# Kernel optimization log

Measured on AMD Instinct MI355X. Metric: run time of the kernel, lower is better.

## Reference

```python
import jax, jax.numpy as jnp
import numpy as np

N0, N1, N2 = 100000, 50000, 25000
E0, E1 = 400000, 200000
H1, D1 = 4, 64   # layer0: 4 heads x 64
H2, D2 = 1, 64   # layer1: 1 head  x 64
SLOPE = 0.2      # DGL GATConv leaky_relu negative_slope


def gat_conv(h_src, h_dst, src, dst, W, attn_l, attn_r, bias, n_dst, heads, d):
    # linear projection (shared between src and dst, as in DGL GATConv)
    f_src = (h_src @ W).reshape(-1, heads, d)   # (N_src, H, D)
    f_dst = (h_dst @ W).reshape(-1, heads, d)   # (N_dst, H, D)
    el = jnp.einsum('nhd,hd->nh', f_src, attn_l)  # (N_src, H)
    er = jnp.einsum('nhd,hd->nh', f_dst, attn_r)  # (N_dst, H)
    e = jax.nn.leaky_relu(el[src] + er[dst], SLOPE)  # (E, H)
    # edge-softmax over incoming edges of each dst node (numerically stable)
    m = jax.ops.segment_max(e, dst, num_segments=n_dst)      # (N_dst, H)
    ee = jnp.exp(e - m[dst])
    s = jax.ops.segment_sum(ee, dst, num_segments=n_dst)
    alpha = ee / s[dst]                                      # (E, H)
    msg = f_src[src] * alpha[:, :, None]                     # (E, H, D)
    out = jax.ops.segment_sum(msg, dst, num_segments=n_dst)  # (N_dst, H, D)
    return out + bias.reshape(1, heads, d)


def setup_inputs() -> dict:
    key = jax.random.key(0)
    ks = jax.random.split(key, 12)
    return {
        'x': jax.random.normal(ks[0], (N0, 256), jnp.float32),
        'e0_src': jax.random.randint(ks[1], (E0,), 0, N0, jnp.int32),
        'e0_dst': jax.random.randint(ks[2], (E0,), 0, N1, jnp.int32),
        'e1_src': jax.random.randint(ks[3], (E1,), 0, N1, jnp.int32),
        'e1_dst': jax.random.randint(ks[4], (E1,), 0, N2, jnp.int32),
        'W1': jax.random.normal(ks[5], (256, H1 * D1), jnp.float32) * 0.06,
        'al1': jax.random.normal(ks[6], (H1, D1), jnp.float32) * 0.1,
        'ar1': jax.random.normal(ks[7], (H1, D1), jnp.float32) * 0.1,
        'b1': jnp.zeros((H1 * D1,), jnp.float32),
        'W2': jax.random.normal(ks[8], (H1 * D1, H2 * D2), jnp.float32) * 0.06,
        'al2': jax.random.normal(ks[9], (H2, D2), jnp.float32) * 0.1,
        'ar2': jax.random.normal(ks[10], (H2, D2), jnp.float32) * 0.1,
        'b2': jnp.zeros((H2 * D2,), jnp.float32),
    }


def reference(x, e0_src, e0_dst, e1_src, e1_dst,
              W1, al1, ar1, b1, W2, al2, ar2, b2):
    # layer 0: block 100k src -> 50k dst; dst nodes are a prefix of src nodes
    h = gat_conv(x, x[:N1], e0_src, e0_dst, W1, al1, ar1, b1, N1, H1, D1)
    h = jax.nn.relu(h).reshape(N1, H1 * D1)   # activation + flatten(1); dropout is identity at eval
    # layer 1 (final): single head, no activation, flatten
    h = gat_conv(h, h[:N2], e1_src, e1_dst, W2, al2, ar2, b2, N2, H2, D2)
    return h.reshape(N2, H2 * D2)
```

## Files before the change

### kernel.cpp

```cpp
#include <hip/hip_runtime.h>
#include <cstddef>
#include <cstdint>

constexpr int cN0 = 100000, cN1 = 50000, cN2 = 25000;
constexpr int cE0 = 400000, cE1 = 200000;
constexpr float SLOPE = 0.2f;

typedef short short8  __attribute__((ext_vector_type(8)));
typedef short short4v __attribute__((ext_vector_type(4)));
typedef float f32x4   __attribute__((ext_vector_type(4)));

__device__ __forceinline__ unsigned short f2bf(float x) {
    union { float f; uint32_t u; } c; c.f = x;
    uint32_t u = c.u + 0x7FFFu + ((c.u >> 16) & 1u);
    return (unsigned short)(u >> 16);
}
__device__ __forceinline__ float bf2f(uint32_t u) {
    union { uint32_t u; float f; } c; c.u = u << 16; return c.f;
}
__device__ __forceinline__ float lrelu(float x) { return x >= 0.f ? x : SLOPE * x; }

__device__ __forceinline__ uint32_t cvtpk(float lo, float hi) {
    uint32_t r;
    asm("v_cvt_pk_bf16_f32 %0, %1, %2" : "=v"(r) : "v"(lo), "v"(hi));
    return r;
}

__device__ __forceinline__ void gload_lds16(const void* g, void* l) {
    __builtin_amdgcn_global_load_lds(
        (const __attribute__((address_space(1))) unsigned int*)g,
        (__attribute__((address_space(3))) unsigned int*)l, 16, 0, 0);
}


__global__ void hist2_kernel(const int* __restrict__ d0, const int* __restrict__ d1,
                             int* __restrict__ cnt0, int* __restrict__ cnt1) {
    int i = blockIdx.x * blockDim.x + threadIdx.x;
    if (i < cE0) atomicAdd(&cnt0[d0[i]], 1);
    int j = i - cE0;
    if (j >= 0 && j < cE1) atomicAdd(&cnt1[d1[j]], 1);
}

__global__ __launch_bounds__(256) void chunk_sum2_kernel(const int* __restrict__ cnt0, int n0,
                                                         const int* __restrict__ cnt1, int n1,
                                                         int* __restrict__ bsum0, int* __restrict__ bsum1,
                                                         int nblk1) {
    const int* cnt = blockIdx.y ? cnt1 : cnt0;
    int n = blockIdx.y ? n1 : n0;
    int* bsum = blockIdx.y ? bsum1 : bsum0;
    if (blockIdx.y && (int)blockIdx.x >= nblk1) return;
    int i = blockIdx.x * 256 + threadIdx.x;
    int v = (i < n) ? cnt[i] : 0;
    #pragma unroll
    for (int o = 32; o; o >>= 1) v += __shfl_xor(v, o);
    __shared__ int ws[4];
    if ((threadIdx.x & 63) == 0) ws[threadIdx.x >> 6] = v;
    __syncthreads();
    if (threadIdx.x == 0) bsum[blockIdx.x] = ws[0] + ws[1] + ws[2] + ws[3];
}

__device__ __forceinline__ int block_exscan(int v, int& total) {
    int lane = threadIdx.x & 63, w = threadIdx.x >> 6;
    int x = v;
    #pragma unroll
    for (int o = 1; o < 64; o <<= 1) { int t = __shfl_up(x, o); if (lane >= o) x += t; }
    __shared__ int ws[4];
    if (lane == 63) ws[w] = x;
    __syncthreads();
    int add = 0;
    #pragma unroll
    for (int i = 0; i < 4; ++i) if (i < w) add += ws[i];
    total = ws[0] + ws[1] + ws[2] + ws[3];
    return add + x - v;
}

__global__ __launch_bounds__(256) void top_scan2_kernel(const int* __restrict__ bsum0, int nblk0,
                                                        const int* __restrict__ bsum1, int nblk1,
                                                        int* __restrict__ boff0, int* __restrict__ boff1,
                                                        int* __restrict__ tot0, int* __restrict__ tot1) {
    int i = threadIdx.x;
    int tot;
    int v = (i < nblk0) ? bsum0[i] : 0;
    int e = block_exscan(v, tot);
    if (i < nblk0) boff0[i] = e;
    if (i == 0) *tot0 = tot;
    __syncthreads();
    v = (i < nblk1) ? bsum1[i] : 0;
    e = block_exscan(v, tot);
    if (i < nblk1) boff1[i] = e;
    if (i == 0) *tot1 = tot;
}

__global__ __launch_bounds__(256) void chunk_scan2_kernel(const int* __restrict__ cnt0, int n0,
                                                          const int* __restrict__ cnt1, int n1,
                                                          const int* __restrict__ boff0, const int* __restrict__ boff1,
                                                          int* __restrict__ offs0, int* __restrict__ cursor0,
                                                          int* __restrict__ offs1, int* __restrict__ cursor1,
                                                          int nblk1) {
    const int* cnt = blockIdx.y ? cnt1 : cnt0;
    const int* boff = blockIdx.y ? boff1 : boff0;
    int* offs = blockIdx.y ? offs1 : offs0;
    int* cursor = blockIdx.y ? cursor1 : cursor0;
    int n = blockIdx.y ? n1 : n0;
    if (blockIdx.y && (int)blockIdx.x >= nblk1) return;
    int i = blockIdx.x * 256 + threadIdx.x;
    int v = (i < n) ? cnt[i] : 0;
    int tot; int e = block_exscan(v, tot) + boff[blockIdx.x];
    if (i < n) { offs[i] = e; cursor[i] = e; }
}

__global__ void scatter2_kernel(const int* __restrict__ s0, const int* __restrict__ d0,
                                const int* __restrict__ s1, const int* __restrict__ d1,
                                int* __restrict__ cursor0, int* __restrict__ srcidx0,
                                int* __restrict__ cursor1, int* __restrict__ srcidx1) {
    int i = blockIdx.x * blockDim.x + threadIdx.x;
    if (i < cE0) { int p = atomicAdd(&cursor0[d0[i]], 1); srcidx0[p] = s0[i]; }
    int j = i - cE0;
    if (j >= 0 && j < cE1) { int p = atomicAdd(&cursor1[d1[j]], 1); srcidx1[p] = s1[j]; }
}

__global__ __launch_bounds__(256) void bf16_transpose2_kernel(const float* __restrict__ W1,
                                                              const float* __restrict__ W2,
                                                              short* __restrict__ bt1,
                                                              short* __restrict__ bt2) {
    int i = blockIdx.x * 256 + threadIdx.x;
    if (i < 256 * 256) {
        int k = i >> 8, n = i & 255;
        bt1[(size_t)n * 256 + k] = (short)f2bf(W1[i]);
    } else {
        int j = i - 256 * 256;
        if (j < 256 * 64) {
            int k = j >> 6, n = j & 63;
            bt2[(size_t)n * 256 + k] = (short)f2bf(W2[j]);
        }
    }
}

__global__ __launch_bounds__(512, 2) void gemm0_breg(
    const float* __restrict__ A, const short* __restrict__ BT,
    unsigned short* __restrict__ C,
    const float* __restrict__ al, const float* __restrict__ ar,
    float* __restrict__ el, float* __restrict__ er,
    int M, int erN)
{
    __shared__ short Bs[256 * 256];

    const int tid = threadIdx.x;
    const int w = tid >> 6;
    const int lane = tid & 63;
    const int ln = lane & 15;
    const int kg = lane >> 4;
    const int m0 = blockIdx.x * 256;

    #pragma unroll
    for (int i = 0; i < 16; ++i) {
        int seg = 2 * (i * 8 + w);
        int r = seg + (lane >> 5);
        int c = (lane & 31) ^ (r & 7);
        gload_lds16(&BT[(size_t)r * 256 + c * 8], &Bs[(size_t)seg * 256]);
    }

    f32x4 acc[2][16];
    #pragma unroll
    for (int mi = 0; mi < 2; ++mi)
        #pragma unroll
        for (int ni = 0; ni < 16; ++ni)
            #pragma unroll
            for (int j = 0; j < 4; ++j) acc[mi][ni][j] = 0.f;

    int r0 = m0 + w * 32 + ln;      if (r0 >= M) r0 = M - 1;
    int r1 = m0 + w * 32 + 16 + ln; if (r1 >= M) r1 = M - 1;
    const float* ap0 = A + (size_t)r0 * 256 + kg * 8;
    const float* ap1 = A + (size_t)r1 * 256 + kg * 8;

    float4 pa[2][2][2];
    auto loadA = [&](int kt, int buf) {
        pa[buf][0][0] = *(const float4*)(ap0 + kt * 32);
        pa[buf][0][1] = *(const float4*)(ap0 + kt * 32 + 4);
        pa[buf][1][0] = *(const float4*)(ap1 + kt * 32);
        pa[buf][1][1] = *(const float4*)(ap1 + kt * 32 + 4);
    };

    loadA(0, 0);
    __syncthreads();

    const int swb = ln & 7;
    #pragma unroll
    for (int kt = 0; kt < 8; ++kt) {
        const int buf = kt & 1;
        if (kt + 1 < 8) loadA(kt + 1, buf ^ 1);
        short8 af[2];
        #pragma unroll
        for (int mi = 0; mi < 2; ++mi) {
            const float4 p0 = pa[buf][mi][0];
            const float4 p1 = pa[buf][mi][1];
            union { uint32_t u[4]; short8 s; } cv;
            cv.u[0] = cvtpk(p0.x, p0.y);
            cv.u[1] = cvtpk(p0.z, p0.w);
            cv.u[2] = cvtpk(p1.x, p1.y);
            cv.u[3] = cvtpk(p1.z, p1.w);
            af[mi] = cv.s;
        }
        #pragma unroll
        for (int ni = 0; ni < 16; ++ni) {
            int row = ni * 16 + ln;
            int pc = (kt * 4 + kg) ^ swb;
            short8 bf = *(const short8*)&Bs[row * 256 + pc * 8];
            acc[0][ni] = __builtin_amdgcn_mfma_f32_16x16x32_bf16(af[0], bf, acc[0][ni], 0, 0, 0);
            acc[1][ni] = __builtin_amdgcn_mfma_f32_16x16x32_bf16(af[1], bf, acc[1][ni], 0, 0, 0);
        }
    }

    float alv[16], arv[16];
    #pragma unroll
    for (int ni = 0; ni < 16; ++ni) {
        alv[ni] = al[ni * 16 + ln];
        arv[ni] = ar[ni * 16 + ln];
    }
    #pragma unroll
    for (int mi = 0; mi < 2; ++mi) {
        #pragma unroll
        for (int j = 0; j < 4; ++j) {
            float pl[4] = {0, 0, 0, 0}, pr[4] = {0, 0, 0, 0};
            #pragma unroll
            for (int ni = 0; ni < 16; ++ni) {
                float v = acc[mi][ni][j];
                pl[ni >> 2] += v * alv[ni];
                pr[ni >> 2] += v * arv[ni];
            }
            #pragma unroll
            for (int h = 0; h < 4; ++h)
                #pragma unroll
                for (int o = 1; o < 16; o <<= 1) {
                    pl[h] += __shfl_xor(pl[h], o);
                    pr[h] += __shfl_xor(pr[h], o);
                }
            int row = m0 + w * 32 + mi * 16 + kg * 4 + j;
            if (row < M) {
                #pragma unroll
                for (int ni = 0; ni < 16; ++ni)
                    C[(size_t)row * 256 + ni * 16 + ln] = f2bf(acc[mi][ni][j]);
                if (ln == 0) {
                    #pragma unroll
                    for (int h = 0; h < 4; ++h) {
                        el[row * 4 + h] = pl[h];
                        if (row < erN) er[row * 4 + h] = pr[h];
                    }
                }
            }
        }
    }
}

template<int BM, int BN, int WR, int WC>
__global__ __launch_bounds__(256) void gemm_bf16_fused(
    const unsigned short* __restrict__ A, const short* __restrict__ BT,
    unsigned short* __restrict__ C,
    const float* __restrict__ al, const float* __restrict__ ar,
    float* __restrict__ el, float* __restrict__ er,
    int M, int K, int nh, int erN)
{
    constexpr int BK = 32;
    constexpr int PITCH = BK + 8;
    constexpr int MI = BM / WR / 16;
    constexpr int NI = BN / WC / 16;
    constexpr int AITB = BM * 4 / 256;
    constexpr int BIT  = BN * 4 / 256;

    __shared__ short As[BM * PITCH];
    __shared__ short Bs[BN * PITCH];

    const int tid = threadIdx.x;
    const int w = tid >> 6;
    const int lane = tid & 63;
    const int ln = lane & 15;
    const int kg = lane >> 4;
    const int wr = w / WC;
    const int wc = w % WC;
    const int m0 = blockIdx.x * BM;
    const int n0 = blockIdx.y * BN;
    const int N = nh * 64;

    f32x4 acc[MI][NI];
    #pragma unroll
    for (int mi = 0; mi < MI; ++mi)
        #pragma unroll
        for (int ni = 0; ni < NI; ++ni)
            #pragma unroll
            for (int j = 0; j < 4; ++j) acc[mi][ni][j] = 0.f;

    short8 aregb[AITB];
    short8 breg[BIT];

    auto loadA = [&](int k0) {
        #pragma unroll
        for (int p = 0; p < AITB; ++p) {
            int slot = tid + p * 256;
            int r = slot >> 2;
            int kq = (slot & 3) * 8;
            int gr = m0 + r;
            short8 v = {};
            if (gr < M) v = *(const short8*)&A[(size_t)gr * K + k0 + kq];
            aregb[p] = v;
        }
    };
    auto loadB = [&](int k0) {
        #pragma unroll
        for (int p = 0; p < BIT; ++p) {
            int slot = tid + p * 256;
            int r = slot >> 2;
            int kq = (slot & 3) * 8;
            breg[p] = *(const short8*)&BT[(size_t)(n0 + r) * K + k0 + kq];
        }
    };
    auto writeLDS = [&]() {
        #pragma unroll
        for (int p = 0; p < AITB; ++p) {
            int slot = tid + p * 256;
            int r = slot >> 2;
            int kq = (slot & 3) * 8;
            *(short8*)&As[r * PITCH + kq] = aregb[p];
        }
        #pragma unroll
        for (int p = 0; p < BIT; ++p) {
            int slot = tid + p * 256;
            int r = slot >> 2;
            int kq = (slot & 3) * 8;
            *(short8*)&Bs[r * PITCH + kq] = breg[p];
        }
    };

    loadA(0); loadB(0);
    const int T = K / BK;
    for (int t = 0; t < T; ++t) {
        writeLDS();
        __syncthreads();
        if (t + 1 < T) { loadA((t + 1) * BK); loadB((t + 1) * BK); }
        short8 af[MI], bf[NI];
        #pragma unroll
        for (int mi = 0; mi < MI; ++mi)
            af[mi] = *(const short8*)&As[(wr * MI * 16 + mi * 16 + ln) * PITCH + kg * 8];
        #pragma unroll
        for (int ni = 0; ni < NI; ++ni)
            bf[ni] = *(const short8*)&Bs[(wc * NI * 16 + ni * 16 + ln) * PITCH + kg * 8];
        #pragma unroll
        for (int mi = 0; mi < MI; ++mi)
            #pragma unroll
            for (int ni = 0; ni < NI; ++ni)
                acc[mi][ni] = __builtin_amdgcn_mfma_f32_16x16x32_bf16(af[mi], bf[ni], acc[mi][ni], 0, 0, 0);
        __syncthreads();
    }

    const int h = (n0 + wc * NI * 16) >> 6;
    float alv[NI], arv[NI];
    #pragma unroll
    for (int ni = 0; ni < NI; ++ni) {
        alv[ni] = al[h * 64 + ni * 16 + ln];
        arv[ni] = ar[h * 64 + ni * 16 + ln];
    }
    #pragma unroll
    for (int mi = 0; mi < MI; ++mi) {
        float pl[4] = {0, 0, 0, 0}, pr[4] = {0, 0, 0, 0};
        #pragma unroll
        for (int ni = 0; ni < NI; ++ni)
            #pragma unroll
            for (int j = 0; j < 4; ++j) {
                float v = acc[mi][ni][j];
                pl[j] += v * alv[ni];
                pr[j] += v * arv[ni];
            }
        #pragma unroll
        for (int j = 0; j < 4; ++j)
            #pragma unroll
            for (int o = 1; o < 16; o <<= 1) {
                pl[j] += __shfl_xor(pl[j], o);
                pr[j] += __shfl_xor(pr[j], o);
            }
        #pragma unroll
        for (int j = 0; j < 4; ++j) {
            int row = m0 + wr * MI * 16 + mi * 16 + kg * 4 + j;
            if (row < M) {
                #pragma unroll
                for (int ni = 0; ni < NI; ++ni)
                    C[(size_t)row * N + n0 + wc * NI * 16 + ni * 16 + ln] = f2bf(acc[mi][ni][j]);
                if (ln == 0) {
                    el[row * nh + h] = pl[j];
                    if (row < erN) er[row * nh + h] = pr[j];
                }
            }
        }
    }
}


__global__ __launch_bounds__(256) void agg0_kernel(const int* __restrict__ offs,
                                                   const int* __restrict__ srcidx,
                                                   const float* __restrict__ el,
                                                   const float* __restrict__ er,
                                                   const unsigned short* __restrict__ fb,
                                                   const float* __restrict__ bias,
                                                   unsigned short* __restrict__ h1b) {
    int w = threadIdx.x >> 6, lane = threadIdx.x & 63;
    int n = blockIdx.x * 4 + w;
    if (n >= cN1) return;
    int beg = offs[n], end = offs[n + 1];

    int h4 = lane & 3, sub = lane >> 2;
    float erA = er[n * 4 + h4];
    float m = -1e30f, s = 0.f;
    for (int i = beg + sub; i < end; i += 16) {
        int sv = srcidx[i];
        float e = lrelu(el[sv * 4 + h4] + erA);
        if (e > m) { s = s * __expf(m - e) + 1.f; m = e; }
        else s += __expf(e - m);
    }
    #pragma unroll
    for (int o = 4; o < 64; o <<= 1) {
        float m2 = __shfl_xor(m, o), s2 = __shfl_xor(s, o);
        float M = fmaxf(m, m2);
        s = s * __expf(m - M) + s2 * __expf(m2 - M);
        m = M;
    }
    float inv = (s > 0.f) ? 1.f / s : 0.f;

    int half = lane >> 5, lcol = lane & 31;
    int hB = lcol >> 3;
    float mB = __shfl(m, hB);
    float invB = __shfl(inv, hB);
    float erB = __shfl(erA, hB);

    float a[8] = {};
    for (int i = beg + half; i < end; i += 2) {
        int sv = srcidx[i];
        float e = lrelu(el[sv * 4 + hB] + erB);
        float p = __expf(e - mB) * invB;
        uint4 v = *(const uint4*)&fb[(size_t)sv * 256 + lcol * 8];
        a[0] = fmaf(bf2f(v.x & 0xffffu), p, a[0]);
        a[1] = fmaf(bf2f(v.x >> 16),     p, a[1]);
        a[2] = fmaf(bf2f(v.y & 0xffffu), p, a[2]);
        a[3] = fmaf(bf2f(v.y >> 16),     p, a[3]);
        a[4] = fmaf(bf2f(v.z & 0xffffu), p, a[4]);
        a[5] = fmaf(bf2f(v.z >> 16),     p, a[5]);
        a[6] = fmaf(bf2f(v.w & 0xffffu), p, a[6]);
        a[7] = fmaf(bf2f(v.w >> 16),     p, a[7]);
    }
    #pragma unroll
    for (int j = 0; j < 8; ++j) a[j] += __shfl_xor(a[j], 32);
    if (half == 0) {
        short8 r;
        #pragma unroll
        for (int j = 0; j < 8; ++j) {
            float o = a[j] + bias[lcol * 8 + j];
            r[j] = (short)f2bf(o > 0.f ? o : 0.f);
        }
        *(short8*)&h1b[(size_t)n * 256 + lcol * 8] = r;
    }
}

__global__ __launch_bounds__(256) void agg1_kernel(const int* __restrict__ offs,
                                                   const int* __restrict__ srcidx,
                                                   const float* __restrict__ el,
                                                   const float* __restrict__ er,
                                                   const unsigned short* __restrict__ f2b,
                                                   const float* __restrict__ bias,
                                                   float* __restrict__ out) {
    int w = threadIdx.x >> 6, lane = threadIdx.x & 63;
    int n = blockIdx.x * 4 + w;
    if (n >= cN2) return;
    int beg = offs[n], end = offs[n + 1];
    float ern = er[n];

    float m = -1e30f, s = 0.f;
    for (int i = beg + lane; i < end; i += 64) {
        float e = lrelu(el[srcidx[i]] + ern);
        if (e > m) { s = s * __expf(m - e) + 1.f; m = e; }
        else s += __expf(e - m);
    }
    #pragma unroll
    for (int o = 1; o < 64; o <<= 1) {
        float m2 = __shfl_xor(m, o), s2 = __shfl_xor(s, o);
        float M = fmaxf(m, m2);
        s = s * __expf(m - M) + s2 * __expf(m2 - M);
        m = M;
    }
    float inv = (s > 0.f) ? 1.f / s : 0.f;

    int q = lane >> 4, lcol = lane & 15;
    float a[4] = {};
    for (int i = beg + q; i < end; i += 4) {
        int sv = srcidx[i];
        float e = lrelu(el[sv] + ern);
        float p = __expf(e - m) * inv;
        uint2 v = *(const uint2*)&f2b[(size_t)sv * 64 + lcol * 4];
        a[0] = fmaf(bf2f(v.x & 0xffffu), p, a[0]);
        a[1] = fmaf(bf2f(v.x >> 16),     p, a[1]);
        a[2] = fmaf(bf2f(v.y & 0xffffu), p, a[2]);
        a[3] = fmaf(bf2f(v.y >> 16),     p, a[3]);
    }
    #pragma unroll
    for (int o = 16; o < 64; o <<= 1)
        #pragma unroll
        for (int j = 0; j < 4; ++j) a[j] += __shfl_xor(a[j], o);
    if (q == 0) {
        float4 b4 = *(const float4*)&bias[lcol * 4];
        float4 r = make_float4(a[0] + b4.x, a[1] + b4.y, a[2] + b4.z, a[3] + b4.w);
        *(float4*)&out[(size_t)n * 64 + lcol * 4] = r;
    }
}


extern "C" void kernel_launch(void* const* d_in, const int* in_sizes, int n_in,
                              void* d_out, int out_size, void* d_ws, size_t ws_size,
                              hipStream_t stream) {
    const float* x      = (const float*)d_in[0];
    const int*   e0_src = (const int*)d_in[1];
    const int*   e0_dst = (const int*)d_in[2];
    const int*   e1_src = (const int*)d_in[3];
    const int*   e1_dst = (const int*)d_in[4];
    const float* W1     = (const float*)d_in[5];
    const float* al1    = (const float*)d_in[6];
    const float* ar1    = (const float*)d_in[7];
    const float* b1     = (const float*)d_in[8];
    const float* W2     = (const float*)d_in[9];
    const float* al2    = (const float*)d_in[10];
    const float* ar2    = (const float*)d_in[11];
    const float* b2     = (const float*)d_in[12];
    float* out = (float*)d_out;

    char* ws = (char*)d_ws;
    size_t off = 0;
    auto alloc = [&](size_t bytes) -> void* {
        void* p = ws + off;
        off = (off + bytes + 255) & ~(size_t)255;
        return p;
    };
    unsigned short* fb  = (unsigned short*)alloc((size_t)cN0 * 256 * 2);
    unsigned short* h1b = (unsigned short*)alloc((size_t)cN1 * 256 * 2);
    unsigned short* f2b = (unsigned short*)alloc((size_t)cN1 * 64 * 2);
    float* el0  = (float*)alloc((size_t)cN0 * 4 * 4);
    float* er0  = (float*)alloc((size_t)cN1 * 4 * 4);
    float* el2  = (float*)alloc((size_t)cN1 * 4);
    float* er2  = (float*)alloc((size_t)cN2 * 4);
    short* bt1  = (short*)alloc((size_t)256 * 256 * 2);
    short* bt2  = (short*)alloc((size_t)64 * 256 * 2);
    int* cntB    = (int*)alloc((size_t)(cN1 + cN2) * 4);
    int* cnt0    = cntB;
    int* cnt1    = cntB + cN1;
    int* offs0   = (int*)alloc((size_t)(cN1 + 1) * 4);
    int* cursor0 = (int*)alloc((size_t)cN1 * 4);
    int* srcidx0 = (int*)alloc((size_t)cE0 * 4);
    int* offs1   = (int*)alloc((size_t)(cN2 + 1) * 4);
    int* cursor1 = (int*)alloc((size_t)cN2 * 4);
    int* srcidx1 = (int*)alloc((size_t)cE1 * 4);
    int* bsum0   = (int*)alloc(256 * 4);
    int* boff0   = (int*)alloc(256 * 4);
    int* bsum1   = (int*)alloc(256 * 4);
    int* boff1   = (int*)alloc(256 * 4);
    (void)ws_size; (void)n_in; (void)in_sizes; (void)out_size;

    const int nblk0 = (cN1 + 255) / 256;
    const int nblk1 = (cN2 + 255) / 256;

    hipMemsetAsync(cntB, 0, (size_t)(cN1 + cN2) * 4, stream);
    hist2_kernel<<<(cE0 + cE1 + 255) / 256, 256, 0, stream>>>(e0_dst, e1_dst, cnt0, cnt1);
    chunk_sum2_kernel<<<dim3(nblk0, 2), 256, 0, stream>>>(cnt0, cN1, cnt1, cN2, bsum0, bsum1, nblk1);
    top_scan2_kernel<<<1, 256, 0, stream>>>(bsum0, nblk0, bsum1, nblk1, boff0, boff1,
                                            offs0 + cN1, offs1 + cN2);
    chunk_scan2_kernel<<<dim3(nblk0, 2), 256, 0, stream>>>(cnt0, cN1, cnt1, cN2, boff0, boff1,
                                                           offs0, cursor0, offs1, cursor1, nblk1);
    scatter2_kernel<<<(cE0 + cE1 + 255) / 256, 256, 0, stream>>>(e0_src, e0_dst, e1_src, e1_dst,
                                                                 cursor0, srcidx0, cursor1, srcidx1);
    bf16_transpose2_kernel<<<(256 * 256 + 256 * 64 + 255) / 256, 256, 0, stream>>>(W1, W2, bt1, bt2);

    gemm0_breg<<<(cN0 + 255) / 256, 512, 0, stream>>>(x, bt1, fb, al1, ar1, el0, er0, cN0, cN1);
    agg0_kernel<<<(cN1 + 3) / 4, 256, 0, stream>>>(offs0, srcidx0, el0, er0, fb, b1, h1b);

    gemm_bf16_fused<128, 64, 4, 1><<<dim3((cN1 + 127) / 128, 1), 256, 0, stream>>>(
        h1b, bt2, f2b, al2, ar2, el2, er2, cN1, 256, 1, cN2);
    agg1_kernel<<<(cN2 + 3) / 4, 256, 0, stream>>>(offs1, srcidx1, el2, er2, f2b, b2, out);
}
```

Baseline: 189.6 us.

## Split layer-0 GEMM across two column halves per row tile

The fused layer-0 projection kernel now has each block compute only 128 of the 256 output columns for a 256-row tile, so the grid doubles. The shared-memory B tile shrinks by half and the accumulator array shrinks too, which allows a higher occupancy hint (4 blocks per CU instead of 2). The attention dot products for el/er are computed per half, two heads each. The cost is that every fp32 row of x is loaded and converted twice, once per half. This relies on the large last-level cache to absorb the second read.

Measured after the change: 207.6 us. 9.5% more time.

```diff
diff --git a/kernel.cpp b/kernel.cpp
--- a/kernel.cpp
+++ b/kernel.cpp
@@ -136,35 +136,38 @@
     }
 }
 
-__global__ __launch_bounds__(512, 2) void gemm0_breg(
+__global__ __launch_bounds__(512, 4) void gemm0_half(
     const float* __restrict__ A, const short* __restrict__ BT,
     unsigned short* __restrict__ C,
     const float* __restrict__ al, const float* __restrict__ ar,
     float* __restrict__ el, float* __restrict__ er,
     int M, int erN)
 {
-    __shared__ short Bs[256 * 256];
+    __shared__ short Bs[128 * 256];
 
     const int tid = threadIdx.x;
     const int w = tid >> 6;
     const int lane = tid & 63;
     const int ln = lane & 15;
     const int kg = lane >> 4;
-    const int m0 = blockIdx.x * 256;
-
-    #pragma unroll
-    for (int i = 0; i < 16; ++i) {
+    const int tile = blockIdx.x >> 1;
+    const int half = blockIdx.x & 1;
+    const int m0 = tile * 256;
+    const int n0 = half * 128;
+
+    #pragma unroll
+    for (int i = 0; i < 8; ++i) {
         int seg = 2 * (i * 8 + w);
         int r = seg + (lane >> 5);
         int c = (lane & 31) ^ (r & 7);
-        gload_lds16(&BT[(size_t)r * 256 + c * 8], &Bs[(size_t)seg * 256]);
-    }
-
-    f32x4 acc[2][16];
+        gload_lds16(&BT[(size_t)(n0 + r) * 256 + c * 8], &Bs[(size_t)seg * 256]);
+    }
+
+    f32x4 acc[2][8];
     #pragma unroll
     for (int mi = 0; mi < 2; ++mi)
         #pragma unroll
-        for (int ni = 0; ni < 16; ++ni)
+        for (int ni = 0; ni < 8; ++ni)
             #pragma unroll
             for (int j = 0; j < 4; ++j) acc[mi][ni][j] = 0.f;
 
@@ -202,7 +205,7 @@
             af[mi] = cv.s;
         }
         #pragma unroll
-        for (int ni = 0; ni < 16; ++ni) {
+        for (int ni = 0; ni < 8; ++ni) {
             int row = ni * 16 + ln;
             int pc = (kt * 4 + kg) ^ swb;
             short8 bf = *(const short8*)&Bs[row * 256 + pc * 8];
@@ -211,40 +214,42 @@
         }
     }
 
-    float alv[16], arv[16];
-    #pragma unroll
-    for (int ni = 0; ni < 16; ++ni) {
-        alv[ni] = al[ni * 16 + ln];
-        arv[ni] = ar[ni * 16 + ln];
+    const int hb = n0 >> 6;
+    float alv[8], arv[8];
+    #pragma unroll
+    for (int ni = 0; ni < 8; ++ni) {
+        int col = n0 + ni * 16 + ln;
+        alv[ni] = al[col];
+        arv[ni] = ar[col];
     }
     #pragma unroll
     for (int mi = 0; mi < 2; ++mi) {
         #pragma unroll
         for (int j = 0; j < 4; ++j) {
-            float pl[4] = {0, 0, 0, 0}, pr[4] = {0, 0, 0, 0};
-            #pragma unroll
-            for (int ni = 0; ni < 16; ++ni) {
+            float pl[2] = {0, 0}, pr[2] = {0, 0};
+            #pragma unroll
+            for (int ni = 0; ni < 8; ++ni) {
                 float v = acc[mi][ni][j];
                 pl[ni >> 2] += v * alv[ni];
                 pr[ni >> 2] += v * arv[ni];
             }
             #pragma unroll
-            for (int h = 0; h < 4; ++h)
+            for (int hh = 0; hh < 2; ++hh)
                 #pragma unroll
                 for (int o = 1; o < 16; o <<= 1) {
-                    pl[h] += __shfl_xor(pl[h], o);
-                    pr[h] += __shfl_xor(pr[h], o);
+                    pl[hh] += __shfl_xor(pl[hh], o);
+                    pr[hh] += __shfl_xor(pr[hh], o);
                 }
             int row = m0 + w * 32 + mi * 16 + kg * 4 + j;
             if (row < M) {
                 #pragma unroll
-                for (int ni = 0; ni < 16; ++ni)
-                    C[(size_t)row * 256 + ni * 16 + ln] = f2bf(acc[mi][ni][j]);
+                for (int ni = 0; ni < 8; ++ni)
+                    C[(size_t)row * 256 + n0 + ni * 16 + ln] = f2bf(acc[mi][ni][j]);
                 if (ln == 0) {
                     #pragma unroll
-                    for (int h = 0; h < 4; ++h) {
-                        el[row * 4 + h] = pl[h];
-                        if (row < erN) er[row * 4 + h] = pr[h];
+                    for (int hh = 0; hh < 2; ++hh) {
+                        el[row * 4 + hb + hh] = pl[hh];
+                        if (row < erN) er[row * 4 + hb + hh] = pr[hh];
                     }
                 }
             }
@@ -572,7 +577,7 @@
                                                                  cursor0, srcidx0, cursor1, srcidx1);
     bf16_transpose2_kernel<<<(256 * 256 + 256 * 64 + 255) / 256, 256, 0, stream>>>(W1, W2, bt1, bt2);
 
-    gemm0_breg<<<(cN0 + 255) / 256, 512, 0, stream>>>(x, bt1, fb, al1, ar1, el0, er0, cN0, cN1);
+    gemm0_half<<<((cN0 + 255) / 256) * 2, 512, 0, stream>>>(x, bt1, fb, al1, ar1, el0, er0, cN0, cN1);
     agg0_kernel<<<(cN1 + 3) / 4, 256, 0, stream>>>(offs0, srcidx0, el0, er0, fb, b1, h1b);
 
     gemm_bf16_fused<128, 64, 4, 1><<<dim3((cN1 + 127) / 128, 1), 256, 0, stream>>>(
```
